# Optimization experiments

Hardware: AMD Instinct MI355X
Metric: run time of the kernel (lower is better)

## Reference

```python
import jax, jax.numpy as jnp
import numpy as np

B, I, O, D, H = 64, 1152, 32, 8, 16
NUM_ITERS = 3


def squash(s, axis=-1, eps=1e-08):
    sq = jnp.sum(s * s, axis=axis, keepdims=True)
    return (sq / (1.0 + sq)) * s / jnp.sqrt(sq + eps)


def setup_inputs() -> dict:
    key = jax.random.key(0)
    k1, k2 = jax.random.split(key)
    u = jax.random.normal(k1, (B, I, D), dtype=jnp.float32)
    weight = jax.random.normal(k2, (I, O, D, H), dtype=jnp.float32) * 0.1
    return {"u": u, "weight": weight}


def reference(u, weight):
    # u_hat: [b, i, o, h]
    u_hat = jnp.einsum('bid,iodh->bioh', u, weight)
    logits = jnp.zeros(u_hat.shape[:3], dtype=u_hat.dtype)

    def body(logits, _):
        coupling = jax.nn.softmax(logits, axis=-1)        # [b,i,o]
        s = jnp.einsum('bio,bioh->boh', coupling, u_hat)  # [b,o,h]
        v = squash(s)                                     # [b,o,h]
        logits = logits + jnp.einsum('boh,bioh->bio', v, u_hat)
        return logits, v

    _, vs = jax.lax.scan(body, logits, None, length=NUM_ITERS)
    return vs[-1]
```

## Files before the change

### kernel.cpp

```cpp
#include <hip/hip_runtime.h>
#include <hip/hip_bf16.h>

#define BB 64
#define II 1152
#define OO 32
#define DD 8
#define HH 16
#define BOH (BB * OO * HH)
#define WTILE (OO * DD * HH)

#define IC   9
#define NIC  128
#define NBB  16
#define NBG  4
#define NJB  4
#define WS   132

__device__ __forceinline__ float row_sum16(float x)
{
    x += __int_as_float(__builtin_amdgcn_update_dpp(
            0, __float_as_int(x), 0x121, 0xF, 0xF, false));
    x += __int_as_float(__builtin_amdgcn_update_dpp(
            0, __float_as_int(x), 0x122, 0xF, 0xF, false));
    x += __int_as_float(__builtin_amdgcn_update_dpp(
            0, __float_as_int(x), 0x124, 0xF, 0xF, false));
    x += __int_as_float(__builtin_amdgcn_update_dpp(
            0, __float_as_int(x), 0x128, 0xF, 0xF, false));
    return x;
}

__device__ __forceinline__ float o_sum32(float x)
{
    float s = row_sum16(x);
    s += __int_as_float(__builtin_amdgcn_ds_swizzle(__float_as_int(s), 0x401F));
    return s;
}

template<int PASS, bool ATOMIC>
__global__ __launch_bounds__(256)
void pass_kernel(const float* __restrict__ u, const float* __restrict__ w,
                 const float* __restrict__ pv0, const float* __restrict__ pv1,
                 float* __restrict__ out)
{
    __shared__ float Wsh[2][OO * WS];

    const int tid   = threadIdx.x;
    const int o     = tid & 31;
    const int hh    = (tid >> 5) & 1;
    const int bq    = tid >> 6;
    const int bbase = blockIdx.y * NBB;
    const int i0    = blockIdx.x * IC;
    const int hofs  = hh * 8;

    float vsum[NJB][8];
    if (PASS >= 1) {
        #pragma unroll
        for (int jb = 0; jb < NJB; jb++) {
            const int b = bbase + bq * NJB + jb;
            const float* p = pv0 + ((b * OO + o) * HH + hofs);
            float4 a = *(const float4*)p;
            float4 c = *(const float4*)(p + 4);
            vsum[jb][0] = a.x; vsum[jb][1] = a.y; vsum[jb][2] = a.z; vsum[jb][3] = a.w;
            vsum[jb][4] = c.x; vsum[jb][5] = c.y; vsum[jb][6] = c.z; vsum[jb][7] = c.w;
            if (PASS == 2) {
                const float* q = pv1 + ((b * OO + o) * HH + hofs);
                float4 a2 = *(const float4*)q;
                float4 c2 = *(const float4*)(q + 4);
                vsum[jb][0] += a2.x; vsum[jb][1] += a2.y; vsum[jb][2] += a2.z; vsum[jb][3] += a2.w;
                vsum[jb][4] += c2.x; vsum[jb][5] += c2.y; vsum[jb][6] += c2.z; vsum[jb][7] += c2.w;
            }
        }
    }

    float sacc[NJB][8];
    #pragma unroll
    for (int jb = 0; jb < NJB; jb++)
        #pragma unroll
        for (int h2 = 0; h2 < 8; h2++) sacc[jb][h2] = 0.f;

    {
        const float* wg = w + (size_t)i0 * WTILE;
        #pragma unroll
        for (int j = 0; j < 4; j++) {
            const int c = tid + j * 256;
            float4 v4 = *(const float4*)(wg + c * 4);
            *(float4*)&Wsh[0][(c >> 5) * WS + (c & 31) * 4] = v4;
        }
    }
    __syncthreads();

    for (int ii = 0; ii < IC; ii++) {
        const float* wcur = Wsh[ii & 1];
        const bool pf = (ii + 1 < IC);
        float4 t0, t1, t2, t3;
        if (pf) {
            const float* wg = w + (size_t)(i0 + ii + 1) * WTILE;
            t0 = *(const float4*)(wg + (tid      ) * 4);
            t1 = *(const float4*)(wg + (tid + 256) * 4);
            t2 = *(const float4*)(wg + (tid + 512) * 4);
            t3 = *(const float4*)(wg + (tid + 768) * 4);
        }

        float us[NJB][8];
        #pragma unroll
        for (int jb = 0; jb < NJB; jb++) {
            const float* ub = u + ((size_t)(bbase + bq * NJB + jb) * II + (i0 + ii)) * DD;
            float4 a = *(const float4*)ub;
            float4 c = *(const float4*)(ub + 4);
            us[jb][0] = a.x; us[jb][1] = a.y; us[jb][2] = a.z; us[jb][3] = a.w;
            us[jb][4] = c.x; us[jb][5] = c.y; us[jb][6] = c.z; us[jb][7] = c.w;
        }

        float uh[NJB][8];
        #pragma unroll
        for (int jb = 0; jb < NJB; jb++)
            #pragma unroll
            for (int h2 = 0; h2 < 8; h2++) uh[jb][h2] = 0.f;
        #pragma unroll
        for (int d = 0; d < DD; d++) {
            const float* wp = &wcur[o * WS + d * HH + hofs];
            float4 wa = *(const float4*)wp;
            float4 wb = *(const float4*)(wp + 4);
            const float wv[8] = {wa.x, wa.y, wa.z, wa.w, wb.x, wb.y, wb.z, wb.w};
            #pragma unroll
            for (int jb = 0; jb < NJB; jb++)
                #pragma unroll
                for (int h2 = 0; h2 < 8; h2++)
                    uh[jb][h2] = fmaf(us[jb][d], wv[h2], uh[jb][h2]);
        }

        float cc[NJB];
        if (PASS == 0) {
            #pragma unroll
            for (int jb = 0; jb < NJB; jb++) cc[jb] = 1.0f / 32.0f;
        } else {
            #pragma unroll
            for (int jb = 0; jb < NJB; jb++) {
                float lg = 0.f;
                #pragma unroll
                for (int h2 = 0; h2 < 8; h2++)
                    lg = fmaf(vsum[jb][h2], uh[jb][h2], lg);
                lg += __shfl_xor(lg, 32, 64);
                const float e = __expf(lg);
                const float se = o_sum32(e);
                cc[jb] = __fdividef(e, se);
            }
        }

        #pragma unroll
        for (int jb = 0; jb < NJB; jb++)
            #pragma unroll
            for (int h2 = 0; h2 < 8; h2++)
                sacc[jb][h2] = fmaf(cc[jb], uh[jb][h2], sacc[jb][h2]);

        if (pf) {
            float* wn = Wsh[(ii + 1) & 1];
            const int c0 = tid, c1 = tid + 256, c2 = tid + 512, c3 = tid + 768;
            *(float4*)&wn[(c0 >> 5) * WS + (c0 & 31) * 4] = t0;
            *(float4*)&wn[(c1 >> 5) * WS + (c1 & 31) * 4] = t1;
            *(float4*)&wn[(c2 >> 5) * WS + (c2 & 31) * 4] = t2;
            *(float4*)&wn[(c3 >> 5) * WS + (c3 & 31) * 4] = t3;
        }
        __syncthreads();
    }

    #pragma unroll
    for (int jb = 0; jb < NJB; jb++) {
        const int b = bbase + bq * NJB + jb;
        if (ATOMIC) {
            float* p = out + ((b * OO + o) * HH + hofs);
            #pragma unroll
            for (int h2 = 0; h2 < 8; h2++) atomicAdd(p + h2, sacc[jb][h2]);
        } else {
            float* p = out + ((size_t)blockIdx.x * BB + b) * (OO * HH) + o * HH + hofs;
            *(float4*)p       = make_float4(sacc[jb][0], sacc[jb][1], sacc[jb][2], sacc[jb][3]);
            *(float4*)(p + 4) = make_float4(sacc[jb][4], sacc[jb][5], sacc[jb][6], sacc[jb][7]);
        }
    }
}

__global__ __launch_bounds__(256)
void reduce_squash_kernel(const float* __restrict__ part, float* __restrict__ v)
{
    const int t = blockIdx.x * blockDim.x + threadIdx.x;
    float acc = 0.f;
    #pragma unroll 16
    for (int ic = 0; ic < NIC; ic++)
        acc += part[(size_t)ic * BOH + t];
    const float sq = row_sum16(acc * acc);
    const float scale = (sq / (1.f + sq)) * rsqrtf(sq + 1e-8f);
    v[t] = acc * scale;
}

__global__ __launch_bounds__(256)
void squash_kernel(const float* __restrict__ s, float* __restrict__ v)
{
    const int t = blockIdx.x * blockDim.x + threadIdx.x;
    if (t >= BB * OO) return;
    const float4* sp = (const float4*)(s + t * HH);
    float4 a = sp[0], b = sp[1], c = sp[2], d = sp[3];
    float sq = a.x*a.x + a.y*a.y + a.z*a.z + a.w*a.w
             + b.x*b.x + b.y*b.y + b.z*b.z + b.w*b.w
             + c.x*c.x + c.y*c.y + c.z*c.z + c.w*c.w
             + d.x*d.x + d.y*d.y + d.z*d.z + d.w*d.w;
    const float scale = (sq / (1.f + sq)) * rsqrtf(sq + 1e-8f);
    a.x *= scale; a.y *= scale; a.z *= scale; a.w *= scale;
    b.x *= scale; b.y *= scale; b.z *= scale; b.w *= scale;
    c.x *= scale; c.y *= scale; c.z *= scale; c.w *= scale;
    d.x *= scale; d.y *= scale; d.z *= scale; d.w *= scale;
    float4* vp = (float4*)(v + t * HH);
    vp[0] = a; vp[1] = b; vp[2] = c; vp[3] = d;
}

extern "C" void kernel_launch(void* const* d_in, const int* in_sizes, int n_in,
                              void* d_out, int out_size, void* d_ws, size_t ws_size,
                              hipStream_t stream)
{
    (void)in_sizes; (void)n_in; (void)out_size;
    const float* u = (const float*)d_in[0];
    const float* w = (const float*)d_in[1];
    float* out = (float*)d_out;

    const size_t need = ((size_t)NIC * BOH + 2 * BOH) * sizeof(float);
    const dim3 grid(NIC, NBG), blk(256);

    if (ws_size >= need) {
        float* part = (float*)d_ws;
        float* v0   = part + (size_t)NIC * BOH;
        float* v1   = v0 + BOH;
        const int rblocks = BOH / 256;

        pass_kernel<0, false><<<grid, blk, 0, stream>>>(u, w, nullptr, nullptr, part);
        reduce_squash_kernel<<<rblocks, 256, 0, stream>>>(part, v0);
        pass_kernel<1, false><<<grid, blk, 0, stream>>>(u, w, v0, nullptr, part);
        reduce_squash_kernel<<<rblocks, 256, 0, stream>>>(part, v1);
        pass_kernel<2, false><<<grid, blk, 0, stream>>>(u, w, v0, v1, part);
        reduce_squash_kernel<<<rblocks, 256, 0, stream>>>(part, out);
    } else {
        float* s0 = (float*)d_ws;
        float* s1 = s0 + BOH;
        float* v0 = s1 + BOH;
        float* v1 = v0 + BOH;
        hipMemsetAsync(d_ws, 0, 2 * BOH * sizeof(float), stream);
        hipMemsetAsync(d_out, 0, BOH * sizeof(float), stream);
        const int sq_blocks = (BB * OO + 255) / 256;

        pass_kernel<0, true><<<grid, blk, 0, stream>>>(u, w, nullptr, nullptr, s0);
        squash_kernel<<<sq_blocks, 256, 0, stream>>>(s0, v0);
        pass_kernel<1, true><<<grid, blk, 0, stream>>>(u, w, v0, nullptr, s1);
        squash_kernel<<<sq_blocks, 256, 0, stream>>>(s1, v1);
        pass_kernel<2, true><<<grid, blk, 0, stream>>>(u, w, v0, v1, out);
        squash_kernel<<<sq_blocks, 256, 0, stream>>>(out, out);
    }
}
```

Baseline: 143.1 us.

## Stage weight tiles via direct global-to-LDS loads with XOR swizzle, vectorize reduce

Weight tiles now go straight from global memory into LDS through global_load_lds, with an XOR swizzle that avoids bank conflicts. This replaces the padded register round-trip, removing register staging and the ds_write instructions. The cross-lane reductions switch to permlane swap builtins where they are available. The reduce/squash kernel now reads float4 and reduces with DPP quad ops. Correctness depends on the async LDS loads being visible after the existing barrier without an explicit vmcnt wait, and on the swizzle mapping matching on both the write and read sides.

```diff
diff --git a/kernel.cpp b/kernel.cpp
--- a/kernel.cpp
+++ b/kernel.cpp
@@ -1,5 +1,4 @@
 #include <hip/hip_runtime.h>
-#include <hip/hip_bf16.h>
 
 #define BB 64
 #define II 1152
@@ -14,26 +13,59 @@
 #define NBB  16
 #define NBG  4
 #define NJB  4
-#define WS   132
+
+template<int CTRL>
+__device__ __forceinline__ float dpp_add(float x)
+{
+    return x + __int_as_float(__builtin_amdgcn_update_dpp(
+            0, __float_as_int(x), CTRL, 0xF, 0xF, false));
+}
 
 __device__ __forceinline__ float row_sum16(float x)
 {
-    x += __int_as_float(__builtin_amdgcn_update_dpp(
-            0, __float_as_int(x), 0x121, 0xF, 0xF, false));
-    x += __int_as_float(__builtin_amdgcn_update_dpp(
-            0, __float_as_int(x), 0x122, 0xF, 0xF, false));
-    x += __int_as_float(__builtin_amdgcn_update_dpp(
-            0, __float_as_int(x), 0x124, 0xF, 0xF, false));
-    x += __int_as_float(__builtin_amdgcn_update_dpp(
-            0, __float_as_int(x), 0x128, 0xF, 0xF, false));
+    x = dpp_add<0x121>(x);
+    x = dpp_add<0x122>(x);
+    x = dpp_add<0x124>(x);
+    x = dpp_add<0x128>(x);
     return x;
 }
 
-__device__ __forceinline__ float o_sum32(float x)
-{
-    float s = row_sum16(x);
-    s += __int_as_float(__builtin_amdgcn_ds_swizzle(__float_as_int(s), 0x401F));
-    return s;
+__device__ __forceinline__ float add_xor32(float x)
+{
+#if __has_builtin(__builtin_amdgcn_permlane32_swap)
+    auto r = __builtin_amdgcn_permlane32_swap(
+        __float_as_uint(x), __float_as_uint(x), false, false);
+    return __uint_as_float(r[0]) + __uint_as_float(r[1]);
+#else
+    return x + __shfl_xor(x, 32, 64);
+#endif
+}
+
+__device__ __forceinline__ float add_xor16(float x)
+{
+#if __has_builtin(__builtin_amdgcn_permlane16_swap)
+    auto r = __builtin_amdgcn_permlane16_swap(
+        __float_as_uint(x), __float_as_uint(x), false, false);
+    return __uint_as_float(r[0]) + __uint_as_float(r[1]);
+#else
+    return x + __int_as_float(__builtin_amdgcn_ds_swizzle(__float_as_int(x), 0x401F));
+#endif
+}
+
+__device__ __forceinline__ int wswz(int f) { return f ^ (((f >> 7) & 7) << 2); }
+
+__device__ __forceinline__ void stage_w_tile(const float* __restrict__ wg,
+                                             float* __restrict__ wn, int tid)
+{
+    #pragma unroll
+    for (int j = 0; j < 4; j++) {
+        const int P = (tid + j * 256) * 4;
+        const int g = wswz(P);
+        __builtin_amdgcn_global_load_lds(
+            (const __attribute__((address_space(1))) void*)(wg + g),
+            (__attribute__((address_space(3))) void*)(wn + P),
+            16, 0, 0);
+    }
 }
 
 template<int PASS, bool ATOMIC>
@@ -42,7 +74,7 @@
                  const float* __restrict__ pv0, const float* __restrict__ pv1,
                  float* __restrict__ out)
 {
-    __shared__ float Wsh[2][OO * WS];
+    __shared__ __align__(16) float Wsh[2][WTILE];
 
     const int tid   = threadIdx.x;
     const int o     = tid & 31;
@@ -51,6 +83,9 @@
     const int bbase = blockIdx.y * NBB;
     const int i0    = blockIdx.x * IC;
     const int hofs  = hh * 8;
+    const int swm   = (o & 7) << 2;
+
+    stage_w_tile(w + (size_t)i0 * WTILE, Wsh[0], tid);
 
     float vsum[NJB][8];
     if (PASS >= 1) {
@@ -78,28 +113,12 @@
         #pragma unroll
         for (int h2 = 0; h2 < 8; h2++) sacc[jb][h2] = 0.f;
 
-    {
-        const float* wg = w + (size_t)i0 * WTILE;
-        #pragma unroll
-        for (int j = 0; j < 4; j++) {
-            const int c = tid + j * 256;
-            float4 v4 = *(const float4*)(wg + c * 4);
-            *(float4*)&Wsh[0][(c >> 5) * WS + (c & 31) * 4] = v4;
-        }
-    }
     __syncthreads();
 
     for (int ii = 0; ii < IC; ii++) {
         const float* wcur = Wsh[ii & 1];
-        const bool pf = (ii + 1 < IC);
-        float4 t0, t1, t2, t3;
-        if (pf) {
-            const float* wg = w + (size_t)(i0 + ii + 1) * WTILE;
-            t0 = *(const float4*)(wg + (tid      ) * 4);
-            t1 = *(const float4*)(wg + (tid + 256) * 4);
-            t2 = *(const float4*)(wg + (tid + 512) * 4);
-            t3 = *(const float4*)(wg + (tid + 768) * 4);
-        }
+        if (ii + 1 < IC)
+            stage_w_tile(w + (size_t)(i0 + ii + 1) * WTILE, Wsh[(ii + 1) & 1], tid);
 
         float us[NJB][8];
         #pragma unroll
@@ -118,9 +137,10 @@
             for (int h2 = 0; h2 < 8; h2++) uh[jb][h2] = 0.f;
         #pragma unroll
         for (int d = 0; d < DD; d++) {
-            const float* wp = &wcur[o * WS + d * HH + hofs];
-            float4 wa = *(const float4*)wp;
-            float4 wb = *(const float4*)(wp + 4);
+            const int ba = (d * HH + hofs    ) ^ swm;
+            const int bb = (d * HH + hofs + 4) ^ swm;
+            float4 wa = *(const float4*)&wcur[o * (DD * HH) + ba];
+            float4 wb = *(const float4*)&wcur[o * (DD * HH) + bb];
             const float wv[8] = {wa.x, wa.y, wa.z, wa.w, wb.x, wb.y, wb.z, wb.w};
             #pragma unroll
             for (int jb = 0; jb < NJB; jb++)
@@ -140,9 +160,9 @@
                 #pragma unroll
                 for (int h2 = 0; h2 < 8; h2++)
                     lg = fmaf(vsum[jb][h2], uh[jb][h2], lg);
-                lg += __shfl_xor(lg, 32, 64);
+                lg = add_xor32(lg);
                 const float e = __expf(lg);
-                const float se = o_sum32(e);
+                const float se = add_xor16(row_sum16(e));
                 cc[jb] = __fdividef(e, se);
             }
         }
@@ -153,14 +173,6 @@
             for (int h2 = 0; h2 < 8; h2++)
                 sacc[jb][h2] = fmaf(cc[jb], uh[jb][h2], sacc[jb][h2]);
 
-        if (pf) {
-            float* wn = Wsh[(ii + 1) & 1];
-            const int c0 = tid, c1 = tid + 256, c2 = tid + 512, c3 = tid + 768;
-            *(float4*)&wn[(c0 >> 5) * WS + (c0 & 31) * 4] = t0;
-            *(float4*)&wn[(c1 >> 5) * WS + (c1 & 31) * 4] = t1;
-            *(float4*)&wn[(c2 >> 5) * WS + (c2 & 31) * 4] = t2;
-            *(float4*)&wn[(c3 >> 5) * WS + (c3 & 31) * 4] = t3;
-        }
         __syncthreads();
     }
 
@@ -180,16 +192,22 @@
 }
 
 __global__ __launch_bounds__(256)
-void reduce_squash_kernel(const float* __restrict__ part, float* __restrict__ v)
-{
-    const int t = blockIdx.x * blockDim.x + threadIdx.x;
-    float acc = 0.f;
+void reduce_squash4_kernel(const float* __restrict__ part, float* __restrict__ v)
+{
+    const int t4 = blockIdx.x * blockDim.x + threadIdx.x;
+    const float4* p = (const float4*)part + t4;
+    float4 acc = make_float4(0.f, 0.f, 0.f, 0.f);
     #pragma unroll 16
-    for (int ic = 0; ic < NIC; ic++)
-        acc += part[(size_t)ic * BOH + t];
-    const float sq = row_sum16(acc * acc);
+    for (int ic = 0; ic < NIC; ic++) {
+        float4 x = p[(size_t)ic * (BOH / 4)];
+        acc.x += x.x; acc.y += x.y; acc.z += x.z; acc.w += x.w;
+    }
+    float sq = acc.x * acc.x + acc.y * acc.y + acc.z * acc.z + acc.w * acc.w;
+    sq = dpp_add<0xB1>(sq);
+    sq = dpp_add<0x4E>(sq);
     const float scale = (sq / (1.f + sq)) * rsqrtf(sq + 1e-8f);
-    v[t] = acc * scale;
+    acc.x *= scale; acc.y *= scale; acc.z *= scale; acc.w *= scale;
+    ((float4*)v)[t4] = acc;
 }
 
 __global__ __launch_bounds__(256)
@@ -228,14 +246,14 @@
         float* part = (float*)d_ws;
         float* v0   = part + (size_t)NIC * BOH;
         float* v1   = v0 + BOH;
-        const int rblocks = BOH / 256;
+        const int rblocks4 = BOH / 4 / 256;
 
         pass_kernel<0, false><<<grid, blk, 0, stream>>>(u, w, nullptr, nullptr, part);
-        reduce_squash_kernel<<<rblocks, 256, 0, stream>>>(part, v0);
+        reduce_squash4_kernel<<<rblocks4, 256, 0, stream>>>(part, v0);
         pass_kernel<1, false><<<grid, blk, 0, stream>>>(u, w, v0, nullptr, part);
-        reduce_squash_kernel<<<rblocks, 256, 0, stream>>>(part, v1);
+        reduce_squash4_kernel<<<rblocks4, 256, 0, stream>>>(part, v1);
         pass_kernel<2, false><<<grid, blk, 0, stream>>>(u, w, v0, v1, part);
-        reduce_squash_kernel<<<rblocks, 256, 0, stream>>>(part, out);
+        reduce_squash4_kernel<<<rblocks4, 256, 0, stream>>>(part, out);
     } else {
         float* s0 = (float*)d_ws;
         float* s1 = s0 + BOH;
```

After: 146.4 us. 2.3% more time.
